# Optimization experiments

Hardware: AMD Instinct MI355X
Metric: run time of the kernel (lower is better)

Reference implementation:

```python
import jax, jax.numpy as jnp
import numpy as np

N, C0, C1 = 8192, 64, 32
P0 = C0 * (C0 + 1) // 2        # 2080 symmetric 0e x 0e pairs
P1 = C1 * (C1 + 1) // 2        # 528 symmetric 1o x 1o pairs -> 0e and 2e
A1 = C1 * (C1 - 1) // 2        # 496 antisymmetric 1o x 1o pairs -> 1e
M0 = C0 + P0 + P1              # 2672 invariant (0e) multiplicities after concat
M1 = C1 + C0 * C1              # 2080 1o multiplicities after concat
NUM_IRREPS = M0 + M1 + A1 + P1 # 5776 total irrep channels (gates)
OUT0, OUT1, OUT1E, OUT2 = 64, 32, 16, 16


def _basis2e():
    # 5 orthonormal (Frobenius) symmetric traceless 3x3 basis matrices: l=2 projection
    s2 = 1.0 / np.sqrt(2.0); s6 = 1.0 / np.sqrt(6.0)
    B = np.zeros((5, 3, 3), np.float32)
    B[0, 0, 1] = B[0, 1, 0] = s2          # xy
    B[1, 1, 2] = B[1, 2, 1] = s2          # yz
    B[2, 0, 2] = B[2, 2, 0] = s2          # xz
    B[3, 0, 0] = s2; B[3, 1, 1] = -s2     # x^2 - y^2
    B[4, 0, 0] = B[4, 1, 1] = -s6; B[4, 2, 2] = 2 * s6  # 2z^2 - x^2 - y^2
    return B


def setup_inputs() -> dict:
    key = jax.random.key(0)
    ks = jax.random.split(key, 8)
    def w(k, shape, fan_in):
        return jax.random.normal(k, shape, jnp.float32) / np.sqrt(fan_in)
    return {
        'x_s': jax.random.normal(ks[0], (N, C0), jnp.float32),
        'x_v': jax.random.normal(ks[1], (N, C1, 3), jnp.float32),
        'mlp_w1': w(ks[2], (M0, M0), M0),
        'mlp_w2': w(ks[3], (M0, NUM_IRREPS), M0),
        'w0': w(ks[4], (M0, OUT0), M0),
        'w1o': w(ks[5], (M1, OUT1), M1),
        'w1e': w(ks[6], (A1, OUT1E), A1),
        'w2e': w(ks[7], (P1, OUT2), P1),
    }


def _forward(x_s, x_v, mlp_w1, mlp_w2, w0, w1o, w1e, w2e):
    n = x_s.shape[0]
    iu0a, iu0b = np.triu_indices(C0)
    c0 = np.where(iu0a == iu0b, 1.0 / np.sqrt(2.0), 1.0).astype(np.float32)
    iu1a, iu1b = np.triu_indices(C1)
    c1 = np.where(iu1a == iu1b, 1.0 / np.sqrt(2.0), 1.0).astype(np.float32)
    ila, ilb = np.triu_indices(C1, k=1)
    B = jnp.asarray(_basis2e())
    # --- tensor square (Clebsch-Gordan contractions) ---
    # 0e x 0e -> 0e (symmetric pairs)
    ss = x_s[:, iu0a] * x_s[:, iu0b] * c0                                   # [n, P0]
    # 1o x 1o symmetric pairs -> 0e (dot) and 2e (sym traceless)
    va, vb = x_v[:, iu1a], x_v[:, iu1b]                                      # [n, P1, 3]
    vv0 = jnp.sum(va * vb, axis=-1) * (c1 / np.sqrt(3.0))                    # [n, P1]
    vv2 = jnp.einsum('npi,npj,kij->npk', va, vb, B) * c1[None, :, None]      # [n, P1, 5]
    # 1o x 1o antisymmetric pairs -> 1e (cross product)
    vv1e = jnp.cross(x_v[:, ila], x_v[:, ilb]) / np.sqrt(2.0)                # [n, A1, 3]
    # 0e x 1o -> 1o
    sv = (x_s[:, :, None, None] * x_v[:, None, :, :]).reshape(n, C0 * C1, 3) # [n, C0*C1, 3]
    # --- concatenate with original features, grouped by irrep ---
    f0 = jnp.concatenate([x_s, ss, vv0], axis=-1)   # [n, M0] invariants
    f1 = jnp.concatenate([x_v, sv], axis=1)         # [n, M1, 3]
    # --- gating MLP on invariants -> one gate per irrep channel ---
    g = jax.nn.silu(f0 @ mlp_w1) @ mlp_w2           # [n, NUM_IRREPS]
    g0 = g[:, :M0]
    g1 = g[:, M0:M0 + M1]
    g1e = g[:, M0 + M1:M0 + M1 + A1]
    g2 = g[:, M0 + M1 + A1:]
    f0 = f0 * g0
    f1 = f1 * g1[:, :, None]
    f1e = vv1e * g1e[:, :, None]
    f2 = vv2 * g2[:, :, None]
    # --- equivariant linear to output irreps (per-l channel mixing) ---
    o0 = f0 @ w0                                    # [n, OUT0]
    o1 = jnp.einsum('nci,co->noi', f1, w1o)         # [n, OUT1, 3]
    o1e = jnp.einsum('nci,co->noi', f1e, w1e)       # [n, OUT1E, 3]
    o2 = jnp.einsum('ncm,co->nom', f2, w2e)         # [n, OUT2, 5]
    return jnp.concatenate([o0, o1.reshape(n, -1), o1e.reshape(n, -1), o2.reshape(n, -1)], axis=-1)


def reference(x_s, x_v, mlp_w1, mlp_w2, w0, w1o, w1e, w2e):
    return _forward(x_s, x_v, mlp_w1, mlp_w2, w0, w1o, w1e, w2e)
```

## Files before the change

kernel.cpp:

```cpp
#include <hip/hip_runtime.h>
#include <hip/hip_bf16.h>
#include <stdint.h>

#define N_ROWS 8192
#define M0C 2672
#define M1C 2080
#define A1C 496
#define P1C 528
#define KP  2688
#define NP2 5888
#define NIR 5776
#define M1P 2112
#define NPAD1 2816

typedef __attribute__((ext_vector_type(8))) _Float16 half8;
typedef __attribute__((ext_vector_type(4))) float floatx4;

__device__ __forceinline__ void async_copy16(const _Float16* g, _Float16* l) {
  __builtin_amdgcn_global_load_lds(
      (__attribute__((address_space(1))) void*)(g),
      (__attribute__((address_space(3))) void*)(l), 16, 0, 0);
}

__global__ __launch_bounds__(256) void transpose_cvt_kernel(
    const float* __restrict__ src, _Float16* __restrict__ dst,
    int srcR, int srcC, int dstC) {
  __shared__ float tile[32][33];
  const int t = threadIdx.x, tx = t & 31, ty = t >> 5;
  const int bx = blockIdx.x, by = blockIdx.y;
#pragma unroll
  for (int i = 0; i < 4; ++i) {
    int sr = bx * 32 + ty + i * 8;
    int sc = by * 32 + tx;
    tile[ty + i * 8][tx] = (sr < srcR && sc < srcC) ? src[(size_t)sr * srcC + sc] : 0.f;
  }
  __syncthreads();
#pragma unroll
  for (int i = 0; i < 4; ++i) {
    int dr = by * 32 + ty + i * 8;
    int dc = bx * 32 + tx;
    dst[(size_t)dr * dstC + dc] = (_Float16)tile[tx][ty + i * 8];
  }
}

__device__ __forceinline__ void triu_ab(int p, int C, int& a, int& b) {
  float fC = (float)C + 0.5f;
  int ai = (int)(fC - sqrtf(fC * fC - 2.0f * (float)p));
  if (ai < 0) ai = 0;
  while (ai > 0 && ai * C - ai * (ai - 1) / 2 > p) --ai;
  while ((ai + 1) * C - (ai + 1) * ai / 2 <= p) ++ai;
  a = ai;
  b = p - (ai * C - ai * (ai - 1) / 2) + ai;
}

__global__ __launch_bounds__(256) void build_f0_kernel(
    const float* __restrict__ xs_g, const float* __restrict__ xv_g,
    _Float16* __restrict__ f0p) {
  __shared__ float xs[64];
  __shared__ float xv[96];
  const int t = threadIdx.x;
  const size_t n = blockIdx.x;
  if (t < 64) xs[t] = xs_g[n * 64 + t];
  else if (t < 160) xv[t - 64] = xv_g[n * 96 + (t - 64)];
  __syncthreads();
  for (int c = t; c < KP; c += 256) {
    float v;
    if (c < 64) {
      v = xs[c];
    } else if (c < 2144) {
      int a, b;
      triu_ab(c - 64, 64, a, b);
      v = xs[a] * xs[b] * ((a == b) ? 0.70710678118654752f : 1.f);
    } else if (c < M0C) {
      int a, b;
      triu_ab(c - 2144, 32, a, b);
      float d = xv[a * 3] * xv[b * 3] + xv[a * 3 + 1] * xv[b * 3 + 1] +
                xv[a * 3 + 2] * xv[b * 3 + 2];
      v = d * ((a == b) ? 0.70710678118654752f : 1.f) * 0.57735026918962576f;
    } else {
      v = 0.f;
    }
    f0p[n * KP + c] = (_Float16)v;
  }
}

template <bool SILU>
__global__ __launch_bounds__(512, 2) void gemm256_kernel(
    const _Float16* __restrict__ A, const _Float16* __restrict__ B,
    _Float16* __restrict__ C, int K, int lda, int ldb, int ldc) {
  __shared__ alignas(16) _Float16 As[4][256 * 32];
  __shared__ alignas(16) _Float16 Bs[4][256 * 32];
  const int tid = threadIdx.x;

  const int ncol = gridDim.x;
  const int id = blockIdx.y * ncol + blockIdx.x;
  const int xcd = id & 7;
  const int j = id >> 3;
  const int hb = j / (2 * ncol);
  const int w = j - hb * 2 * ncol;
  const int by = xcd * 4 + hb * 2 + (w & 1);
  const int bx = w >> 1;
  const size_t row0 = (size_t)by * 256;
  const size_t col0 = (size_t)bx * 256;

  const _Float16 *pA0, *pA1, *pB0, *pB1;
  _Float16 *lA0, *lA1, *lB0, *lB1;
  {
    int c0 = tid, c1 = tid + 512;
    int r0 = c0 >> 2, ch0 = c0 & 3;
    int r1 = c1 >> 2, ch1 = c1 & 3;
    int s0 = ch0 ^ ((r0 >> 1) & 3);
    int s1 = ch1 ^ ((r1 >> 1) & 3);
    pA0 = A + (row0 + r0) * lda + s0 * 8;
    pA1 = A + (row0 + r1) * lda + s1 * 8;
    pB0 = B + (col0 + r0) * ldb + s0 * 8;
    pB1 = B + (col0 + r1) * ldb + s1 * 8;
    lA0 = &As[0][c0 * 8]; lA1 = &As[0][c1 * 8];
    lB0 = &Bs[0][c0 * 8]; lB1 = &Bs[0][c1 * 8];
  }

  const int lane = tid & 63;
  const int wv = tid >> 6;
  const int wm = wv & 1;
  const int wn = wv >> 1;
  const int m16 = lane & 15;
  const int quad = lane >> 4;
  const int sw8 = (quad ^ ((m16 >> 1) & 3)) * 8;
  const int aoff = (wm * 128 + m16) * 32 + sw8;
  const int boff = (wn * 64 + m16) * 32 + sw8;

  floatx4 acc[8][4] = {};

#define STAGE(BB)                                             \
  {                                                           \
    async_copy16(pA0, lA0 + (BB) * (256 * 32));               \
    async_copy16(pA1, lA1 + (BB) * (256 * 32));               \
    async_copy16(pB0, lB0 + (BB) * (256 * 32));               \
    async_copy16(pB1, lB1 + (BB) * (256 * 32));               \
    pA0 += 32; pA1 += 32; pB0 += 32; pB1 += 32;               \
  }

#define COMPUTE(BB)                                                           \
  {                                                                           \
    half8 bf[4], af[4];                                                       \
    _Pragma("unroll")                                                         \
    for (int jj = 0; jj < 4; ++jj)                                            \
      bf[jj] = *(const half8*)&Bs[BB][boff + jj * 512];                       \
    _Pragma("unroll")                                                         \
    for (int ii = 0; ii < 4; ++ii)                                            \
      af[ii] = *(const half8*)&As[BB][aoff + ii * 512];                       \
    __builtin_amdgcn_s_setprio(1);                                            \
    _Pragma("unroll")                                                         \
    for (int ii = 0; ii < 4; ++ii)                                            \
      _Pragma("unroll")                                                       \
      for (int jj = 0; jj < 4; ++jj)                                          \
        acc[ii][jj] = __builtin_amdgcn_mfma_f32_16x16x32_f16(                 \
            af[ii], bf[jj], acc[ii][jj], 0, 0, 0);                            \
    __builtin_amdgcn_s_setprio(0);                                            \
    _Pragma("unroll")                                                         \
    for (int ii = 0; ii < 4; ++ii)                                            \
      af[ii] = *(const half8*)&As[BB][aoff + (ii + 4) * 512];                 \
    __builtin_amdgcn_s_setprio(1);                                            \
    _Pragma("unroll")                                                         \
    for (int ii = 0; ii < 4; ++ii)                                            \
      _Pragma("unroll")                                                       \
      for (int jj = 0; jj < 4; ++jj)                                          \
        acc[ii + 4][jj] = __builtin_amdgcn_mfma_f32_16x16x32_f16(             \
            af[ii], bf[jj], acc[ii + 4][jj], 0, 0, 0);                        \
    __builtin_amdgcn_s_setprio(0);                                            \
    asm volatile("s_waitcnt lgkmcnt(0)" ::: "memory");                        \
  }

#define KITER(BB, DO_STAGE, VMLIT)                               \
  {                                                              \
    if (DO_STAGE) STAGE(((BB) + 2) & 3);                         \
    asm volatile("s_waitcnt vmcnt(" VMLIT ")" ::: "memory");     \
    __builtin_amdgcn_s_barrier();                                \
    asm volatile("" ::: "memory");                               \
    COMPUTE(BB);                                                 \
  }

  STAGE(0);
  STAGE(1);
  const int T = K >> 5;
  for (int t4 = 0; t4 + 4 < T; t4 += 4) {
    KITER(0, 1, "8");
    KITER(1, 1, "8");
    KITER(2, 1, "8");
    KITER(3, 1, "8");
  }
  KITER(0, 1, "8");
  KITER(1, 1, "8");
  KITER(2, 0, "4");
  KITER(3, 0, "0");
#undef KITER
#undef COMPUTE
#undef STAGE

#pragma unroll
  for (int ii = 0; ii < 8; ++ii) {
    size_t r = row0 + wm * 128 + ii * 16 + quad * 4;
#pragma unroll
    for (int jj = 0; jj < 4; ++jj) {
      size_t cc = col0 + wn * 64 + jj * 16 + m16;
#pragma unroll
      for (int rr = 0; rr < 4; ++rr) {
        float v = acc[ii][jj][rr];
        if (SILU) v = v / (1.f + __expf(-v));
        C[(r + rr) * ldc + cc] = (_Float16)v;
      }
    }
  }
}

__global__ __launch_bounds__(256) void epi0_kernel(
    const _Float16* __restrict__ f0p, const _Float16* __restrict__ G,
    const _Float16* __restrict__ w0T, float* __restrict__ out) {
  __shared__ alignas(16) _Float16 As[32 * 64];
  const int t = threadIdx.x;
  const size_t n0 = (size_t)blockIdx.x * 32;
  const int lane = t & 63, wave = t >> 6;
  const int m16 = lane & 15, quad = lane >> 4;
  const int rt = (wave & 1) * 16;
  const int ctb = (wave >> 1) * 32;
  const int br = t >> 3, p = t & 7;
  const int l8 = (p ^ (br & 7)) * 8;

  floatx4 acc[2] = {};
  for (int k0 = 0; k0 < KP; k0 += 64) {
    if (k0) __syncthreads();
    {
      half8 f = *(const half8*)&f0p[(n0 + br) * KP + k0 + l8];
      half8 g = *(const half8*)&G[(n0 + br) * NP2 + k0 + l8];
      half8 a;
#pragma unroll
      for (int j = 0; j < 8; ++j) a[j] = (_Float16)((float)f[j] * (float)g[j]);
      *(half8*)&As[br * 64 + p * 8] = a;
    }
    __syncthreads();
#pragma unroll
    for (int kk = 0; kk < 2; ++kk) {
      int q = kk * 4 + quad;
      half8 af = *(const half8*)&As[(rt + m16) * 64 + (q ^ (m16 & 7)) * 8];
#pragma unroll
      for (int c = 0; c < 2; ++c) {
        half8 bf = *(const half8*)&w0T[(size_t)(ctb + c * 16 + m16) * KP + k0 + kk * 32 + quad * 8];
        acc[c] = __builtin_amdgcn_mfma_f32_16x16x32_f16(af, bf, acc[c], 0, 0, 0);
      }
    }
  }
#pragma unroll
  for (int c = 0; c < 2; ++c)
#pragma unroll
    for (int rr = 0; rr < 4; ++rr)
      out[(n0 + rt + quad * 4 + rr) * 288 + ctb + c * 16 + m16] = acc[c][rr];
}

__global__ __launch_bounds__(256) void epi1_kernel(
    const float* __restrict__ xs_g, const float* __restrict__ xv_g,
    const _Float16* __restrict__ G, const _Float16* __restrict__ w1oT,
    float* __restrict__ out) {
  __shared__ float xs[32][64];
  __shared__ float xv[32][96];
  __shared__ alignas(16) _Float16 As[3][32 * 64];
  const int t = threadIdx.x;
  const size_t n0 = (size_t)blockIdx.x * 32;
  for (int idx = t; idx < 32 * 64; idx += 256)
    xs[idx >> 6][idx & 63] = xs_g[(n0 + (idx >> 6)) * 64 + (idx & 63)];
  for (int idx = t; idx < 32 * 96; idx += 256)
    xv[idx / 96][idx % 96] = xv_g[(n0 + idx / 96) * 96 + idx % 96];
  const int lane = t & 63, wave = t >> 6;
  const int m16 = lane & 15, quad = lane >> 4;
  const int rt = (wave & 1) * 16;
  const int ct = (wave >> 1) * 16;
  const int br = t >> 3, p = t & 7;
  const int l8 = (p ^ (br & 7)) * 8;

  floatx4 acc[3] = {};
  __syncthreads();
  for (int k0 = 0; k0 < M1P; k0 += 64) {
    if (k0) __syncthreads();
    {
      half8 g8 = *(const half8*)&G[(n0 + br) * NP2 + M0C + k0 + l8];
      int kbase = k0 + l8;
      half8 a0, a1, a2;
      if (kbase < 32) {
#pragma unroll
        for (int j = 0; j < 8; ++j) {
          float g = (float)g8[j];
          int v = kbase + j;
          a0[j] = (_Float16)(xv[br][v * 3 + 0] * g);
          a1[j] = (_Float16)(xv[br][v * 3 + 1] * g);
          a2[j] = (_Float16)(xv[br][v * 3 + 2] * g);
        }
      } else {
        int s = (kbase - 32) >> 5;
        if (s > 63) s = 63;
        int v0 = (kbase - 32) & 31;
        float xsr = xs[br][s];
#pragma unroll
        for (int j = 0; j < 8; ++j) {
          float g = (float)g8[j] * xsr;
          int v = v0 + j;
          a0[j] = (_Float16)(xv[br][v * 3 + 0] * g);
          a1[j] = (_Float16)(xv[br][v * 3 + 1] * g);
          a2[j] = (_Float16)(xv[br][v * 3 + 2] * g);
        }
      }
      *(half8*)&As[0][br * 64 + p * 8] = a0;
      *(half8*)&As[1][br * 64 + p * 8] = a1;
      *(half8*)&As[2][br * 64 + p * 8] = a2;
    }
    __syncthreads();
#pragma unroll
    for (int kk = 0; kk < 2; ++kk) {
      int q = kk * 4 + quad;
      half8 bf = *(const half8*)&w1oT[(size_t)(ct + m16) * M1P + k0 + kk * 32 + quad * 8];
#pragma unroll
      for (int i = 0; i < 3; ++i) {
        half8 af = *(const half8*)&As[i][(rt + m16) * 64 + (q ^ (m16 & 7)) * 8];
        acc[i] = __builtin_amdgcn_mfma_f32_16x16x32_f16(af, bf, acc[i], 0, 0, 0);
      }
    }
  }
#pragma unroll
  for (int i = 0; i < 3; ++i)
#pragma unroll
    for (int rr = 0; rr < 4; ++rr)
      out[(n0 + rt + quad * 4 + rr) * 288 + 64 + (ct + m16) * 3 + i] = acc[i][rr];
}

__global__ __launch_bounds__(256) void epi1e2_kernel(
    const float* __restrict__ xv_g, const _Float16* __restrict__ G,
    const _Float16* __restrict__ w1eT, const _Float16* __restrict__ w2eT,
    float* __restrict__ out) {
  __shared__ float xv[64][96];
  __shared__ alignas(16) _Float16 As[5][64 * 32];
  __shared__ uint8_t pa[544], pb[544];
  const int t = threadIdx.x;
  const size_t n0 = (size_t)blockIdx.x * 64;
  const int phase = blockIdx.y;
  for (int idx = t; idx < 64 * 96; idx += 256)
    xv[idx / 96][idx % 96] = xv_g[(n0 + idx / 96) * 96 + idx % 96];
  for (int p = t; p < 544; p += 256) {
    int a = 0, b = 0;
    if (phase == 0) {
      if (p < A1C) { triu_ab(p, 31, a, b); b += 1; }
    } else {
      if (p < P1C) triu_ab(p, 32, a, b);
    }
    pa[p] = (uint8_t)a; pb[p] = (uint8_t)b;
  }
  const int lane = t & 63, wave = t >> 6;
  const int m16 = lane & 15, quad = lane >> 4;
  const int sw8 = (quad ^ ((m16 >> 1) & 3)) * 8;
  const int br = t >> 2;
  const int bc8 = ((t & 3) ^ ((br >> 1) & 3)) * 8;
  const int lc8 = (t & 3) * 8;
  const float s2 = 0.70710678118654752f, s6 = 0.40824829046386302f;
  __syncthreads();

  if (phase == 0) {
    floatx4 acc[3] = {};
    for (int k0 = 0; k0 < 512; k0 += 32) {
      if (k0) __syncthreads();
      {
        half8 g8 = *(const half8*)&G[(n0 + br) * NP2 + (M0C + M1C) + k0 + bc8];
        half8 a0, a1, a2;
#pragma unroll
        for (int j = 0; j < 8; ++j) {
          int p = k0 + bc8 + j;
          if (p < A1C) {
            int a = pa[p], b = pb[p];
            float ax = xv[br][a * 3], ay = xv[br][a * 3 + 1], az = xv[br][a * 3 + 2];
            float bx = xv[br][b * 3], by = xv[br][b * 3 + 1], bz = xv[br][b * 3 + 2];
            float g = (float)g8[j] * s2;
            a0[j] = (_Float16)((ay * bz - az * by) * g);
            a1[j] = (_Float16)((az * bx - ax * bz) * g);
            a2[j] = (_Float16)((ax * by - ay * bx) * g);
          } else {
            a0[j] = (_Float16)0.f; a1[j] = (_Float16)0.f; a2[j] = (_Float16)0.f;
          }
        }
        *(half8*)&As[0][br * 32 + lc8] = a0;
        *(half8*)&As[1][br * 32 + lc8] = a1;
        *(half8*)&As[2][br * 32 + lc8] = a2;
      }
      __syncthreads();
      half8 bf = *(const half8*)&w1eT[(size_t)m16 * 512 + k0 + quad * 8];
#pragma unroll
      for (int i = 0; i < 3; ++i) {
        half8 af = *(const half8*)&As[i][(wave * 16 + m16) * 32 + sw8];
        acc[i] = __builtin_amdgcn_mfma_f32_16x16x32_f16(af, bf, acc[i], 0, 0, 0);
      }
    }
#pragma unroll
    for (int i = 0; i < 3; ++i)
#pragma unroll
      for (int rr = 0; rr < 4; ++rr)
        out[(n0 + wave * 16 + quad * 4 + rr) * 288 + 160 + m16 * 3 + i] = acc[i][rr];
  } else {
    floatx4 acc[5] = {};
    for (int k0 = 0; k0 < 544; k0 += 32) {
      if (k0) __syncthreads();
      {
        half8 g8 = *(const half8*)&G[(n0 + br) * NP2 + (M0C + M1C + A1C) + k0 + bc8];
        half8 m0v, m1v, m2v, m3v, m4v;
#pragma unroll
        for (int j = 0; j < 8; ++j) {
          int p = k0 + bc8 + j;
          if (p < P1C) {
            int a = pa[p], b = pb[p];
            float ax = xv[br][a * 3], ay = xv[br][a * 3 + 1], az = xv[br][a * 3 + 2];
            float bx = xv[br][b * 3], by = xv[br][b * 3 + 1], bz = xv[br][b * 3 + 2];
            float c1 = (a == b) ? s2 : 1.f;
            float gw = (float)g8[j] * c1;
            m0v[j] = (_Float16)(s2 * (ax * by + ay * bx) * gw);
            m1v[j] = (_Float16)(s2 * (ay * bz + az * by) * gw);
            m2v[j] = (_Float16)(s2 * (ax * bz + az * bx) * gw);
            m3v[j] = (_Float16)(s2 * (ax * bx - ay * by) * gw);
            m4v[j] = (_Float16)(s6 * (2.f * az * bz - ax * bx - ay * by) * gw);
          } else {
            m0v[j] = (_Float16)0.f; m1v[j] = (_Float16)0.f; m2v[j] = (_Float16)0.f;
            m3v[j] = (_Float16)0.f; m4v[j] = (_Float16)0.f;
          }
        }
        *(half8*)&As[0][br * 32 + lc8] = m0v;
        *(half8*)&As[1][br * 32 + lc8] = m1v;
        *(half8*)&As[2][br * 32 + lc8] = m2v;
        *(half8*)&As[3][br * 32 + lc8] = m3v;
        *(half8*)&As[4][br * 32 + lc8] = m4v;
      }
      __syncthreads();
      half8 bf = *(const half8*)&w2eT[(size_t)m16 * 544 + k0 + quad * 8];
#pragma unroll
      for (int m = 0; m < 5; ++m) {
        half8 af = *(const half8*)&As[m][(wave * 16 + m16) * 32 + sw8];
        acc[m] = __builtin_amdgcn_mfma_f32_16x16x32_f16(af, bf, acc[m], 0, 0, 0);
      }
    }
#pragma unroll
    for (int m = 0; m < 5; ++m)
#pragma unroll
      for (int rr = 0; rr < 4; ++rr)
        out[(n0 + wave * 16 + quad * 4 + rr) * 288 + 208 + m16 * 5 + m] = acc[m][rr];
  }
}

extern "C" void kernel_launch(void* const* d_in, const int* in_sizes, int n_in,
                              void* d_out, int out_size, void* d_ws, size_t ws_size,
                              hipStream_t stream) {
  const float* xs  = (const float*)d_in[0];
  const float* xv  = (const float*)d_in[1];
  const float* w1  = (const float*)d_in[2];
  const float* w2  = (const float*)d_in[3];
  const float* w0  = (const float*)d_in[4];
  const float* w1o = (const float*)d_in[5];
  const float* w1e = (const float*)d_in[6];
  const float* w2e = (const float*)d_in[7];
  float* out = (float*)d_out;

  char* ws = (char*)d_ws;
  size_t off = 0;
  _Float16* w1T = (_Float16*)(ws + off); off += (size_t)NPAD1 * KP * 2;
  _Float16* w2T = (_Float16*)(ws + off); off += (size_t)NP2 * KP * 2;
  _Float16* f0p = (_Float16*)(ws + off); off += (size_t)N_ROWS * KP * 2;
  _Float16* H   = (_Float16*)(ws + off); off += (size_t)N_ROWS * NPAD1 * 2;
  _Float16* G   = (_Float16*)(ws + off);

  _Float16* w0T  = w1T;
  _Float16* w1oT = (_Float16*)((char*)w1T + 344064);
  _Float16* w1eT = (_Float16*)((char*)w1T + 479232);
  _Float16* w2eT = (_Float16*)((char*)w1T + 512000);

  transpose_cvt_kernel<<<dim3(KP / 32, NPAD1 / 32), 256, 0, stream>>>(w1, w1T, M0C, M0C, KP);
  transpose_cvt_kernel<<<dim3(KP / 32, NP2 / 32), 256, 0, stream>>>(w2, w2T, M0C, NIR, KP);
  build_f0_kernel<<<N_ROWS, 256, 0, stream>>>(xs, xv, f0p);
  gemm256_kernel<true><<<dim3(NPAD1 / 256, N_ROWS / 256), 512, 0, stream>>>(
      f0p, w1T, H, KP, KP, KP, NPAD1);
  transpose_cvt_kernel<<<dim3(KP / 32, 2), 256, 0, stream>>>(w0, w0T, M0C, 64, KP);
  transpose_cvt_kernel<<<dim3(M1P / 32, 1), 256, 0, stream>>>(w1o, w1oT, M1C, 32, M1P);
  transpose_cvt_kernel<<<dim3(16, 1), 256, 0, stream>>>(w1e, w1eT, A1C, 16, 512);
  transpose_cvt_kernel<<<dim3(17, 1), 256, 0, stream>>>(w2e, w2eT, P1C, 16, 544);
  gemm256_kernel<false><<<dim3(NP2 / 256, N_ROWS / 256), 512, 0, stream>>>(
      H, w2T, G, KP, NPAD1, KP, NP2);
  epi0_kernel<<<256, 256, 0, stream>>>(f0p, G, w0T, out);
  epi1_kernel<<<256, 256, 0, stream>>>(xs, xv, G, w1oT, out);
  epi1e2_kernel<<<dim3(128, 2), 256, 0, stream>>>(xv, G, w1eT, w2eT, out);
}
```

Measured before the change: 740.2 us.

## Deepen GEMM prefetch to three stages and preload next tile's LDS fragments

The 256x256 fp16 MFMA GEMM now keeps three global->LDS stages in flight instead of two. Inside each k-iteration it reads the second half of the A fragments and the next buffer's A/B fragments from LDS before the MFMA block, using double-buffered register sets and sched_barriers so those LDS reads overlap the matrix math. The aim is to hide both global-load and LDS-read latency behind MFMAs. It costs more VGPRs, which could cause spills under launch_bounds(512,2), and the LDS ring now has less slack against buffer reuse races.

```diff
diff --git a/kernel.cpp b/kernel.cpp
--- a/kernel.cpp
+++ b/kernel.cpp
@@ -88,8 +88,8 @@
 __global__ __launch_bounds__(512, 2) void gemm256_kernel(
     const _Float16* __restrict__ A, const _Float16* __restrict__ B,
     _Float16* __restrict__ C, int K, int lda, int ldb, int ldc) {
-  __shared__ alignas(16) _Float16 As[4][256 * 32];
-  __shared__ alignas(16) _Float16 Bs[4][256 * 32];
+  __shared__ alignas(16) _Float16 As[4 * 256 * 32];
+  __shared__ alignas(16) _Float16 Bs[4 * 256 * 32];
   const int tid = threadIdx.x;
 
   const int ncol = gridDim.x;
@@ -115,8 +115,8 @@
     pA1 = A + (row0 + r1) * lda + s1 * 8;
     pB0 = B + (col0 + r0) * ldb + s0 * 8;
     pB1 = B + (col0 + r1) * ldb + s1 * 8;
-    lA0 = &As[0][c0 * 8]; lA1 = &As[0][c1 * 8];
-    lB0 = &Bs[0][c0 * 8]; lB1 = &Bs[0][c1 * 8];
+    lA0 = &As[c0 * 8]; lA1 = &As[c1 * 8];
+    lB0 = &Bs[c0 * 8]; lB1 = &Bs[c1 * 8];
   }
 
   const int lane = tid & 63;
@@ -133,68 +133,75 @@
 
 #define STAGE(BB)                                             \
   {                                                           \
-    async_copy16(pA0, lA0 + (BB) * (256 * 32));               \
-    async_copy16(pA1, lA1 + (BB) * (256 * 32));               \
-    async_copy16(pB0, lB0 + (BB) * (256 * 32));               \
-    async_copy16(pB1, lB1 + (BB) * (256 * 32));               \
+    async_copy16(pA0, lA0 + (BB) * 8192);                     \
+    async_copy16(pA1, lA1 + (BB) * 8192);                     \
+    async_copy16(pB0, lB0 + (BB) * 8192);                     \
+    async_copy16(pB1, lB1 + (BB) * 8192);                     \
     pA0 += 32; pA1 += 32; pB0 += 32; pB1 += 32;               \
   }
 
-#define COMPUTE(BB)                                                           \
+#define KITER(BB, CAA, CBF, CAB, NAA, NBF, VMLIT, DO_STAGE, DO_READN)         \
   {                                                                           \
-    half8 bf[4], af[4];                                                       \
-    _Pragma("unroll")                                                         \
-    for (int jj = 0; jj < 4; ++jj)                                            \
-      bf[jj] = *(const half8*)&Bs[BB][boff + jj * 512];                       \
+    if (DO_STAGE) STAGE(((BB) + 3) & 3);                                      \
+    asm volatile("s_waitcnt vmcnt(" VMLIT ")" ::: "memory");                  \
+    __builtin_amdgcn_s_barrier();                                             \
+    __builtin_amdgcn_sched_barrier(0);                                        \
     _Pragma("unroll")                                                         \
     for (int ii = 0; ii < 4; ++ii)                                            \
-      af[ii] = *(const half8*)&As[BB][aoff + ii * 512];                       \
+      CAB[ii] = *(const half8*)&As[(BB) * 8192 + aoff + (ii + 4) * 512];      \
+    if (DO_READN) {                                                           \
+      _Pragma("unroll")                                                       \
+      for (int jj = 0; jj < 4; ++jj)                                          \
+        NBF[jj] = *(const half8*)&Bs[(((BB) + 1) & 3) * 8192 + boff + jj * 512]; \
+      _Pragma("unroll")                                                       \
+      for (int ii = 0; ii < 4; ++ii)                                          \
+        NAA[ii] = *(const half8*)&As[(((BB) + 1) & 3) * 8192 + aoff + ii * 512]; \
+    }                                                                         \
+    __builtin_amdgcn_sched_barrier(0);                                        \
     __builtin_amdgcn_s_setprio(1);                                            \
     _Pragma("unroll")                                                         \
     for (int ii = 0; ii < 4; ++ii)                                            \
       _Pragma("unroll")                                                       \
       for (int jj = 0; jj < 4; ++jj)                                          \
         acc[ii][jj] = __builtin_amdgcn_mfma_f32_16x16x32_f16(                 \
-            af[ii], bf[jj], acc[ii][jj], 0, 0, 0);                            \
+            CAA[ii], CBF[jj], acc[ii][jj], 0, 0, 0);                          \
     __builtin_amdgcn_s_setprio(0);                                            \
-    _Pragma("unroll")                                                         \
-    for (int ii = 0; ii < 4; ++ii)                                            \
-      af[ii] = *(const half8*)&As[BB][aoff + (ii + 4) * 512];                 \
+    __builtin_amdgcn_sched_barrier(0);                                        \
     __builtin_amdgcn_s_setprio(1);                                            \
     _Pragma("unroll")                                                         \
     for (int ii = 0; ii < 4; ++ii)                                            \
       _Pragma("unroll")                                                       \
       for (int jj = 0; jj < 4; ++jj)                                          \
         acc[ii + 4][jj] = __builtin_amdgcn_mfma_f32_16x16x32_f16(             \
-            af[ii], bf[jj], acc[ii + 4][jj], 0, 0, 0);                        \
+            CAB[ii], CBF[jj], acc[ii + 4][jj], 0, 0, 0);                      \
     __builtin_amdgcn_s_setprio(0);                                            \
     asm volatile("s_waitcnt lgkmcnt(0)" ::: "memory");                        \
   }
 
-#define KITER(BB, DO_STAGE, VMLIT)                               \
-  {                                                              \
-    if (DO_STAGE) STAGE(((BB) + 2) & 3);                         \
-    asm volatile("s_waitcnt vmcnt(" VMLIT ")" ::: "memory");     \
-    __builtin_amdgcn_s_barrier();                                \
-    asm volatile("" ::: "memory");                               \
-    COMPUTE(BB);                                                 \
-  }
-
   STAGE(0);
   STAGE(1);
+  STAGE(2);
+  asm volatile("s_waitcnt vmcnt(8)" ::: "memory");
+  __builtin_amdgcn_s_barrier();
+  __builtin_amdgcn_sched_barrier(0);
+  half8 aA0[4], bF0[4], aB0[4], aA1[4], bF1[4], aB1[4];
+#pragma unroll
+  for (int jj = 0; jj < 4; ++jj) bF0[jj] = *(const half8*)&Bs[boff + jj * 512];
+#pragma unroll
+  for (int ii = 0; ii < 4; ++ii) aA0[ii] = *(const half8*)&As[aoff + ii * 512];
+
   const int T = K >> 5;
-  for (int t4 = 0; t4 + 4 < T; t4 += 4) {
-    KITER(0, 1, "8");
-    KITER(1, 1, "8");
-    KITER(2, 1, "8");
-    KITER(3, 1, "8");
-  }
-  KITER(0, 1, "8");
-  KITER(1, 1, "8");
-  KITER(2, 0, "4");
-  KITER(3, 0, "0");
+  for (int t4 = 0; t4 < T - 4; t4 += 4) {
+    KITER(0, aA0, bF0, aB0, aA1, bF1, "8", 1, 1);
+    KITER(1, aA1, bF1, aB1, aA0, bF0, "8", 1, 1);
+    KITER(2, aA0, bF0, aB0, aA1, bF1, "8", 1, 1);
+    KITER(3, aA1, bF1, aB1, aA0, bF0, "8", 1, 1);
+  }
+  KITER(0, aA0, bF0, aB0, aA1, bF1, "8", 1, 1);
+  KITER(1, aA1, bF1, aB1, aA0, bF0, "4", 0, 1);
+  KITER(2, aA0, bF0, aB0, aA1, bF1, "0", 0, 1);
+  KITER(3, aA1, bF1, aB1, aA0, bF0, "0", 0, 0);
 #undef KITER
-#undef COMPUTE
 #undef STAGE
 
 #pragma unroll
```

New measurement: 736.2 us. Within noise of the previous version (-0.5%).

## Split GEMM k-iteration into two barriered phases interleaving LDS reads and async loads

Applied to the files above, without the earlier changes.

Restructures the 256x256 fp16 GEMM main loop so each k-step runs as two phases. The A-tile prefetch is issued in the first phase and the B-tile prefetch in the second, and each phase is fenced by scheduling barriers and workgroup barriers. The goal is to overlap LDS fragment reads and global-to-LDS copies with the MFMA bursts more evenly across waves. The cost is twice as many s_barrier calls per k-step and tighter vmcnt waits, which could add stalls.

```diff
diff --git a/kernel.cpp b/kernel.cpp
--- a/kernel.cpp
+++ b/kernel.cpp
@@ -88,8 +88,8 @@
 __global__ __launch_bounds__(512, 2) void gemm256_kernel(
     const _Float16* __restrict__ A, const _Float16* __restrict__ B,
     _Float16* __restrict__ C, int K, int lda, int ldb, int ldc) {
-  __shared__ alignas(16) _Float16 As[4][256 * 32];
-  __shared__ alignas(16) _Float16 Bs[4][256 * 32];
+  __shared__ alignas(16) _Float16 As[4 * 8192];
+  __shared__ alignas(16) _Float16 Bs[4 * 8192];
   const int tid = threadIdx.x;
 
   const int ncol = gridDim.x;
@@ -115,8 +115,8 @@
     pA1 = A + (row0 + r1) * lda + s1 * 8;
     pB0 = B + (col0 + r0) * ldb + s0 * 8;
     pB1 = B + (col0 + r1) * ldb + s1 * 8;
-    lA0 = &As[0][c0 * 8]; lA1 = &As[0][c1 * 8];
-    lB0 = &Bs[0][c0 * 8]; lB1 = &Bs[0][c1 * 8];
+    lA0 = &As[c0 * 8]; lA1 = &As[c1 * 8];
+    lB0 = &Bs[c0 * 8]; lB1 = &Bs[c1 * 8];
   }
 
   const int lane = tid & 63;
@@ -130,25 +130,34 @@
   const int boff = (wn * 64 + m16) * 32 + sw8;
 
   floatx4 acc[8][4] = {};
-
-#define STAGE(BB)                                             \
-  {                                                           \
-    async_copy16(pA0, lA0 + (BB) * (256 * 32));               \
-    async_copy16(pA1, lA1 + (BB) * (256 * 32));               \
-    async_copy16(pB0, lB0 + (BB) * (256 * 32));               \
-    async_copy16(pB1, lB1 + (BB) * (256 * 32));               \
-    pA0 += 32; pA1 += 32; pB0 += 32; pB1 += 32;               \
-  }
-
-#define COMPUTE(BB)                                                           \
+  half8 af[4], bf[4];
+
+#define STAGE_A(SLOT)                                 \
+  {                                                   \
+    async_copy16(pA0, lA0 + (SLOT) * 8192);           \
+    async_copy16(pA1, lA1 + (SLOT) * 8192);           \
+    pA0 += 32; pA1 += 32;                             \
+  }
+#define STAGE_B(SLOT)                                 \
+  {                                                   \
+    async_copy16(pB0, lB0 + (SLOT) * 8192);           \
+    async_copy16(pB1, lB1 + (SLOT) * 8192);           \
+    pB0 += 32; pB1 += 32;                             \
+  }
+
+#define PH0(BB, DO_STAGE)                                                     \
   {                                                                           \
-    half8 bf[4], af[4];                                                       \
+    _Pragma("unroll")                                                         \
+    for (int ii = 0; ii < 4; ++ii)                                            \
+      af[ii] = *(const half8*)&As[(BB) * 8192 + aoff + ii * 512];             \
     _Pragma("unroll")                                                         \
     for (int jj = 0; jj < 4; ++jj)                                            \
-      bf[jj] = *(const half8*)&Bs[BB][boff + jj * 512];                       \
-    _Pragma("unroll")                                                         \
-    for (int ii = 0; ii < 4; ++ii)                                            \
-      af[ii] = *(const half8*)&As[BB][aoff + ii * 512];                       \
+      bf[jj] = *(const half8*)&Bs[(BB) * 8192 + boff + jj * 512];             \
+    if (DO_STAGE) STAGE_A(((BB) + 2) & 3);                                    \
+    __builtin_amdgcn_sched_barrier(0);                                        \
+    __builtin_amdgcn_s_barrier();                                             \
+    asm volatile("s_waitcnt lgkmcnt(0)" ::: "memory");                        \
+    __builtin_amdgcn_sched_barrier(0);                                        \
     __builtin_amdgcn_s_setprio(1);                                            \
     _Pragma("unroll")                                                         \
     for (int ii = 0; ii < 4; ++ii)                                            \
@@ -157,9 +166,21 @@
         acc[ii][jj] = __builtin_amdgcn_mfma_f32_16x16x32_f16(                 \
             af[ii], bf[jj], acc[ii][jj], 0, 0, 0);                            \
     __builtin_amdgcn_s_setprio(0);                                            \
+    __builtin_amdgcn_sched_barrier(0);                                        \
+    __builtin_amdgcn_s_barrier();                                             \
+  }
+
+#define PH1(BB, DO_STAGE, VMLIT)                                              \
+  {                                                                           \
     _Pragma("unroll")                                                         \
     for (int ii = 0; ii < 4; ++ii)                                            \
-      af[ii] = *(const half8*)&As[BB][aoff + (ii + 4) * 512];                 \
+      af[ii] = *(const half8*)&As[(BB) * 8192 + aoff + (ii + 4) * 512];       \
+    if (DO_STAGE) STAGE_B(((BB) + 2) & 3);                                    \
+    asm volatile("s_waitcnt vmcnt(" VMLIT ")" ::: "memory");                  \
+    __builtin_amdgcn_sched_barrier(0);                                        \
+    __builtin_amdgcn_s_barrier();                                             \
+    asm volatile("s_waitcnt lgkmcnt(0)" ::: "memory");                        \
+    __builtin_amdgcn_sched_barrier(0);                                        \
     __builtin_amdgcn_s_setprio(1);                                            \
     _Pragma("unroll")                                                         \
     for (int ii = 0; ii < 4; ++ii)                                            \
@@ -168,34 +189,30 @@
         acc[ii + 4][jj] = __builtin_amdgcn_mfma_f32_16x16x32_f16(             \
             af[ii], bf[jj], acc[ii + 4][jj], 0, 0, 0);                        \
     __builtin_amdgcn_s_setprio(0);                                            \
-    asm volatile("s_waitcnt lgkmcnt(0)" ::: "memory");                        \
-  }
-
-#define KITER(BB, DO_STAGE, VMLIT)                               \
-  {                                                              \
-    if (DO_STAGE) STAGE(((BB) + 2) & 3);                         \
-    asm volatile("s_waitcnt vmcnt(" VMLIT ")" ::: "memory");     \
-    __builtin_amdgcn_s_barrier();                                \
-    asm volatile("" ::: "memory");                               \
-    COMPUTE(BB);                                                 \
-  }
-
-  STAGE(0);
-  STAGE(1);
+    __builtin_amdgcn_sched_barrier(0);                                        \
+    __builtin_amdgcn_s_barrier();                                             \
+  }
+
+  STAGE_A(0); STAGE_B(0);
+  STAGE_A(1); STAGE_B(1);
+  asm volatile("s_waitcnt vmcnt(4)" ::: "memory");
+  __builtin_amdgcn_s_barrier();
+
   const int T = K >> 5;
-  for (int t4 = 0; t4 + 4 < T; t4 += 4) {
-    KITER(0, 1, "8");
-    KITER(1, 1, "8");
-    KITER(2, 1, "8");
-    KITER(3, 1, "8");
-  }
-  KITER(0, 1, "8");
-  KITER(1, 1, "8");
-  KITER(2, 0, "4");
-  KITER(3, 0, "0");
-#undef KITER
-#undef COMPUTE
-#undef STAGE
+  for (int t4 = 0; t4 < T - 4; t4 += 4) {
+    PH0(0, 1); PH1(0, 1, "4");
+    PH0(1, 1); PH1(1, 1, "4");
+    PH0(2, 1); PH1(2, 1, "4");
+    PH0(3, 1); PH1(3, 1, "4");
+  }
+  PH0(0, 1); PH1(0, 1, "4");
+  PH0(1, 1); PH1(1, 1, "4");
+  PH0(2, 0); PH1(2, 0, "0");
+  PH0(3, 0); PH1(3, 0, "0");
+#undef PH1
+#undef PH0
+#undef STAGE_B
+#undef STAGE_A
 
 #pragma unroll
   for (int ii = 0; ii < 8; ++ii) {
```

Result: slower. 759.9 us (+2.7%).
